# Optimization experiments

Measured on AMD Instinct MI355X. Metric: run time of the kernel, lower is better.

Reference implementation:

```python
import jax, jax.numpy as jnp
import numpy as np

N_NODES = 50000
N_EDGES = 800000
N_GRAPHS = 256
N_FEAT, N_HID, N_EMB = 128, 256, 256
BN_EPS = 1e-5
W_SCALE = 0.05  # keep activations well-scaled through 3 layers


def setup_inputs() -> dict:
    key = jax.random.key(0)
    ks = jax.random.split(key, 9)
    x = jax.random.normal(ks[0], (N_NODES, N_FEAT), jnp.float32)
    edge_index = jax.random.randint(ks[1], (2, N_EDGES), 0, N_NODES)
    batch = jnp.sort(jax.random.randint(ks[2], (N_NODES,), 0, N_GRAPHS))
    return {
        "x": x,
        "edge_index": edge_index,
        "batch": batch,
        "W1_0": jax.random.normal(ks[3], (N_FEAT, N_HID), jnp.float32) * W_SCALE,
        "W2_0": jax.random.normal(ks[4], (N_HID, N_HID), jnp.float32) * W_SCALE,
        "gamma0": jnp.ones((N_HID,), jnp.float32),
        "beta0": jnp.zeros((N_HID,), jnp.float32),
        "W1_1": jax.random.normal(ks[5], (N_HID, N_HID), jnp.float32) * W_SCALE,
        "W2_1": jax.random.normal(ks[6], (N_HID, N_HID), jnp.float32) * W_SCALE,
        "gamma1": jnp.ones((N_HID,), jnp.float32),
        "beta1": jnp.zeros((N_HID,), jnp.float32),
        "W1_2": jax.random.normal(ks[7], (N_HID, N_HID), jnp.float32) * W_SCALE,
        "W2_2": jax.random.normal(ks[8], (N_HID, N_EMB), jnp.float32) * W_SCALE,
    }


def _gin_conv(x, src, dst, W1, W2):
    # PyG GINConv, eps=0: nn((1+eps)*x_i + sum_{j in N(i)} x_j)
    agg = jax.ops.segment_sum(x[src], dst, num_segments=N_NODES)  # [N, d]
    h = x + agg
    return jax.nn.relu(h @ W1) @ W2  # Linear(bias=False) -> act -> Linear(bias=False)


def _batch_norm(h, gamma, beta):
    # BatchNorm1d in training mode: biased batch stats over nodes
    mean = jnp.mean(h, axis=0)
    var = jnp.var(h, axis=0)
    return (h - mean) * jax.lax.rsqrt(var + BN_EPS) * gamma + beta


def reference(x, edge_index, batch, W1_0, W2_0, gamma0, beta0,
              W1_1, W2_1, gamma1, beta1, W1_2, W2_2):
    src, dst = edge_index[0], edge_index[1]
    layers = [(W1_0, W2_0, gamma0, beta0), (W1_1, W2_1, gamma1, beta1)]
    xs = []
    h = x
    for W1, W2, g, b in layers:  # n_layers-1 conv+act+BN blocks
        h = jax.nn.relu(_gin_conv(h, src, dst, W1, W2))
        h = _batch_norm(h, g, b)
        xs.append(h)
    h = _gin_conv(h, src, dst, W1_2, W2_2)  # final conv: no act, no BN
    xs.append(h)
    xpool = jax.ops.segment_sum(h, batch, num_segments=N_GRAPHS)  # global_add_pool
    return xpool, jnp.concatenate(xs, axis=1)
```

## Files before the change

### kernel.cpp

```cpp
#include <hip/hip_runtime.h>
#include <stdint.h>

typedef unsigned int u32;
typedef unsigned short u16;

using s16x8 = __attribute__((ext_vector_type(8))) short;
using f32x4 = __attribute__((ext_vector_type(4))) float;

#define N_NODES_C 50000
#define N_EDGES_C 800000
#define N_GRAPHS_C 256
#define N_FEAT_C 128
#define N_HID_C 256

static __device__ __forceinline__ float bf2f(u16 u) {
  union { u32 u; float f; } c; c.u = ((u32)u) << 16; return c.f;
}
static __device__ __forceinline__ u16 f2bf(float f) {
  union { float f; u32 u; } c; c.f = f;
  u32 u = c.u;
  return (u16)((u + 0x7fffu + ((u >> 16) & 1u)) >> 16);
}

static __device__ __forceinline__ void gload_lds16(const u16* g, u16* l) {
  __builtin_amdgcn_global_load_lds(
      (const __attribute__((address_space(1))) unsigned int*)g,
      (__attribute__((address_space(3))) unsigned int*)l, 16, 0, 0);
}

__global__ void convt_all_kernel(const float* __restrict__ Wa, const float* __restrict__ Wb,
                                 const float* __restrict__ Wc, const float* __restrict__ Wd,
                                 const float* __restrict__ We, const float* __restrict__ Wf,
                                 u16* oa, u16* ob, u16* oc, u16* od, u16* oe, u16* of_) {
  int m = blockIdx.y;
  const float* W; u16* o; int K;
  switch (m) {
    case 0: W = Wa; o = oa; K = 128; break;
    case 1: W = Wb; o = ob; K = 256; break;
    case 2: W = Wc; o = oc; K = 256; break;
    case 3: W = Wd; o = od; K = 256; break;
    case 4: W = We; o = oe; K = 256; break;
    default: W = Wf; o = of_; K = 256; break;
  }
  int idx = blockIdx.x * 256 + threadIdx.x;
  if (idx >= K * 256) return;
  int n = idx / K, k = idx - n * K;
  o[idx] = f2bf(W[(size_t)k * 256 + n]);
}

__global__ void cvt4_kernel(const float* __restrict__ x, u16* __restrict__ xb, int n4) {
  int idx = blockIdx.x * 256 + threadIdx.x;
  if (idx >= n4) return;
  float4 v = reinterpret_cast<const float4*>(x)[idx];
  u32 lo = (u32)f2bf(v.x) | ((u32)f2bf(v.y) << 16);
  u32 hi = (u32)f2bf(v.z) | ((u32)f2bf(v.w) << 16);
  uint2 w; w.x = lo; w.y = hi;
  reinterpret_cast<uint2*>(xb)[idx] = w;
}

__global__ void count_kernel(const int* __restrict__ dst, int* __restrict__ cnt, int E) {
  int e = blockIdx.x * 256 + threadIdx.x;
  if (e < E) atomicAdd(&cnt[dst[e]], 1);
}

__global__ void scanA_kernel(const int* __restrict__ cnt, int* __restrict__ incl,
                             int* __restrict__ bsum, int n) {
  __shared__ int sd[1024];
  int i = blockIdx.x * 1024 + (int)threadIdx.x;
  int v = (i < n) ? cnt[i] : 0;
  sd[threadIdx.x] = v;
  __syncthreads();
  for (int off = 1; off < 1024; off <<= 1) {
    int t = ((int)threadIdx.x >= off) ? sd[threadIdx.x - off] : 0;
    __syncthreads();
    sd[threadIdx.x] += t;
    __syncthreads();
  }
  if (i < n) incl[i] = sd[threadIdx.x];
  if (threadIdx.x == 1023) bsum[blockIdx.x] = sd[1023];
}

__global__ void scanB_kernel(int* bsum, int nb, float* stats0, float* stats1) {
  int t = threadIdx.x;
  for (int i = t; i < 512; i += 64) { stats0[i] = 0.f; stats1[i] = 0.f; }
  if (t == 0) {
    int s = 0;
    for (int b = 0; b < nb; b++) { int v = bsum[b]; bsum[b] = s; s += v; }
  }
}

__global__ void scanC_kernel(const int* __restrict__ cnt, const int* __restrict__ incl,
                             const int* __restrict__ bsum, int* __restrict__ offs,
                             int* __restrict__ cursor, int n) {
  int i = blockIdx.x * 1024 + (int)threadIdx.x;
  if (i < n) {
    int e = incl[i] - cnt[i] + bsum[blockIdx.x];
    offs[i] = e;
    cursor[i] = e;
  }
  if (i == 0) offs[n] = N_EDGES_C;
}

__global__ void fill_kernel(const int* __restrict__ src, const int* __restrict__ dst,
                            int* __restrict__ cursor, int* __restrict__ csr, int E) {
  int e = blockIdx.x * 256 + threadIdx.x;
  if (e < E) {
    int p = atomicAdd(&cursor[dst[e]], 1);
    csr[p] = src[e];
  }
}

template <int D, bool AFFINE>
__global__ __launch_bounds__(256) void agg_kernel(const u16* __restrict__ xin,
                                                  const int* __restrict__ offs,
                                                  const int* __restrict__ csr,
                                                  const float* __restrict__ sb,
                                                  u16* __restrict__ hout) {
  constexpr int LPE = D / 8;
  constexpr int EPW = 64 / LPE;
  int wid = threadIdx.x >> 6, lane = threadIdx.x & 63;
  int node = blockIdx.x * 4 + wid;
  if (node >= N_NODES_C) return;
  int sub = lane / LPE;
  int fl = lane % LPE;
  int f0 = fl * 8;
  float acc[8];
  if (sub == 0) {
    uint4 v = *reinterpret_cast<const uint4*>(xin + (size_t)node * D + f0);
    const u32* pv = reinterpret_cast<const u32*>(&v);
#pragma unroll
    for (int t = 0; t < 4; t++) {
      acc[2 * t] = bf2f((u16)pv[t]);
      acc[2 * t + 1] = bf2f((u16)(pv[t] >> 16));
    }
  } else {
#pragma unroll
    for (int t = 0; t < 8; t++) acc[t] = 0.f;
  }
  int e0 = offs[node];
  int e1 = offs[node + 1];
  int e = e0 + sub;
  if (EPW == 2) {
    for (; e + 3 * EPW < e1; e += 4 * EPW) {
      int s0 = csr[e], s1 = csr[e + EPW], s2 = csr[e + 2 * EPW], s3 = csr[e + 3 * EPW];
      uint4 v0 = *reinterpret_cast<const uint4*>(xin + (size_t)s0 * D + f0);
      uint4 v1 = *reinterpret_cast<const uint4*>(xin + (size_t)s1 * D + f0);
      uint4 v2 = *reinterpret_cast<const uint4*>(xin + (size_t)s2 * D + f0);
      uint4 v3 = *reinterpret_cast<const uint4*>(xin + (size_t)s3 * D + f0);
      const u32* p0 = reinterpret_cast<const u32*>(&v0);
      const u32* p1 = reinterpret_cast<const u32*>(&v1);
      const u32* p2 = reinterpret_cast<const u32*>(&v2);
      const u32* p3 = reinterpret_cast<const u32*>(&v3);
#pragma unroll
      for (int t = 0; t < 4; t++) {
        acc[2 * t] += (bf2f((u16)p0[t]) + bf2f((u16)p1[t])) +
                      (bf2f((u16)p2[t]) + bf2f((u16)p3[t]));
        acc[2 * t + 1] += (bf2f((u16)(p0[t] >> 16)) + bf2f((u16)(p1[t] >> 16))) +
                          (bf2f((u16)(p2[t] >> 16)) + bf2f((u16)(p3[t] >> 16)));
      }
    }
  } else {
    for (; e + EPW < e1; e += 2 * EPW) {
      int s0 = csr[e], s1 = csr[e + EPW];
      uint4 v0 = *reinterpret_cast<const uint4*>(xin + (size_t)s0 * D + f0);
      uint4 v1 = *reinterpret_cast<const uint4*>(xin + (size_t)s1 * D + f0);
      const u32* p0 = reinterpret_cast<const u32*>(&v0);
      const u32* p1 = reinterpret_cast<const u32*>(&v1);
#pragma unroll
      for (int t = 0; t < 4; t++) {
        acc[2 * t] += bf2f((u16)p0[t]) + bf2f((u16)p1[t]);
        acc[2 * t + 1] += bf2f((u16)(p0[t] >> 16)) + bf2f((u16)(p1[t] >> 16));
      }
    }
  }
  for (; e < e1; e += EPW) {
    int s = csr[e];
    uint4 v = *reinterpret_cast<const uint4*>(xin + (size_t)s * D + f0);
    const u32* pv = reinterpret_cast<const u32*>(&v);
#pragma unroll
    for (int t = 0; t < 4; t++) {
      acc[2 * t] += bf2f((u16)pv[t]);
      acc[2 * t + 1] += bf2f((u16)(pv[t] >> 16));
    }
  }
#pragma unroll
  for (int j = 0; j < 8; j++) {
    if (EPW == 4) acc[j] += __shfl_xor(acc[j], 16, 64);
    acc[j] += __shfl_xor(acc[j], 32, 64);
  }
  if (sub == 0) {
    if (AFFINE) {
      float dp1 = (float)(e1 - e0 + 1);
      float4 sca = *reinterpret_cast<const float4*>(sb + f0);
      float4 scb = *reinterpret_cast<const float4*>(sb + f0 + 4);
      float4 bia = *reinterpret_cast<const float4*>(sb + 256 + f0);
      float4 bib = *reinterpret_cast<const float4*>(sb + 256 + f0 + 4);
      float sc[8] = {sca.x, sca.y, sca.z, sca.w, scb.x, scb.y, scb.z, scb.w};
      float bi[8] = {bia.x, bia.y, bia.z, bia.w, bib.x, bib.y, bib.z, bib.w};
#pragma unroll
      for (int j = 0; j < 8; j++) acc[j] = fmaf(acc[j], sc[j], bi[j] * dp1);
    }
    u32 w[4];
#pragma unroll
    for (int t = 0; t < 4; t++)
      w[t] = (u32)f2bf(acc[2 * t]) | ((u32)f2bf(acc[2 * t + 1]) << 16);
    *reinterpret_cast<uint4*>(hout + (size_t)node * D + f0) =
        *reinterpret_cast<const uint4*>(w);
  }
}

template <int K, bool RELU, bool OUTF32, bool STATS>
__global__ __launch_bounds__(512, 2) void gemm_kernel(const u16* __restrict__ A,
                                                      const u16* __restrict__ Bt,
                                                      u16* __restrict__ outB,
                                                      float* __restrict__ outF, int ldc,
                                                      float* __restrict__ statsp) {
  constexpr int BM = 128, BK = 64;
  __shared__ u16 Al[BM * BK];
  __shared__ u16 Bl[256 * BK];
  const int tid = threadIdx.x;
  const int wid = tid >> 6, lane = tid & 63;
  const int brow = blockIdx.x * BM;
  const int wr = (wid >> 2) * 64;
  const int wc = (wid & 3) * 64;
  f32x4 acc[4][4] = {};

  const int lrow = lane >> 3;
  const int lw = lane & 7;
  const int colA = (lw ^ lrow) * 8;
  const int sw = (lane & 7) << 3;

  for (int k0 = 0; k0 < K; k0 += BK) {
#pragma unroll
    for (int i = 0; i < 6; i++) {
      int c = wid * 6 + i;
      if (c < 16) {
        int r = c * 8 + lrow;
        int gr = brow + r;
        gr = gr < N_NODES_C ? gr : N_NODES_C - 1;
        gload_lds16(A + (size_t)gr * K + k0 + colA, &Al[c * 512]);
      } else {
        int cc = c - 16;
        int r = cc * 8 + lrow;
        gload_lds16(Bt + (size_t)r * K + k0 + colA, &Bl[cc * 512]);
      }
    }
    __syncthreads();
#pragma unroll
    for (int ks = 0; ks < BK; ks += 32) {
      const int kk = ks + (lane >> 4) * 8;
      const int ki = kk ^ sw;
      s16x8 a[4], b[4];
#pragma unroll
      for (int m = 0; m < 4; m++)
        a[m] = *reinterpret_cast<const s16x8*>(&Al[(wr + m * 16 + (lane & 15)) * 64 + ki]);
#pragma unroll
      for (int n = 0; n < 4; n++)
        b[n] = *reinterpret_cast<const s16x8*>(&Bl[(wc + n * 16 + (lane & 15)) * 64 + ki]);
#pragma unroll
      for (int m = 0; m < 4; m++)
#pragma unroll
        for (int n = 0; n < 4; n++)
          acc[m][n] = __builtin_amdgcn_mfma_f32_16x16x32_bf16(a[m], b[n], acc[m][n], 0, 0, 0);
    }
    __syncthreads();
  }

  const int cb = wc + (lane & 15);
  const int rsub = (lane >> 4) * 4;
  float s1[4] = {0.f, 0.f, 0.f, 0.f}, s2[4] = {0.f, 0.f, 0.f, 0.f};
#pragma unroll
  for (int m = 0; m < 4; m++) {
#pragma unroll
    for (int r = 0; r < 4; r++) {
      int row = brow + wr + m * 16 + rsub + r;
      if (row >= N_NODES_C) continue;
#pragma unroll
      for (int n = 0; n < 4; n++) {
        float v = acc[m][n][r];
        if (RELU) v = v > 0.f ? v : 0.f;
        int col = cb + n * 16;
        if (OUTF32)
          outF[(size_t)row * ldc + col] = v;
        else
          outB[(size_t)row * ldc + col] = f2bf(v);
        if (STATS) { s1[n] += v; s2[n] += v * v; }
      }
    }
  }
  if (STATS) {
#pragma unroll
    for (int n = 0; n < 4; n++) {
      float a0 = s1[n], b0 = s2[n];
      a0 += __shfl_xor(a0, 16, 64);
      b0 += __shfl_xor(b0, 16, 64);
      a0 += __shfl_xor(a0, 32, 64);
      b0 += __shfl_xor(b0, 32, 64);
      if (lane < 16) {
        atomicAdd(&statsp[cb + n * 16], a0);
        atomicAdd(&statsp[256 + cb + n * 16], b0);
      }
    }
  }
}

__global__ __launch_bounds__(256) void norm_kernel(const u16* __restrict__ xp,
                                                   const float* __restrict__ stats,
                                                   const float* __restrict__ gamma,
                                                   const float* __restrict__ beta,
                                                   float* __restrict__ cout,
                                                   float* __restrict__ sb) {
  const float invM = 1.0f / (float)N_NODES_C;
  int f0 = (threadIdx.x & 127) * 2;
  int half = threadIdx.x >> 7;
  float m0 = stats[f0] * invM, m1 = stats[f0 + 1] * invM;
  float v0 = stats[256 + f0] * invM - m0 * m0;
  float v1 = stats[256 + f0 + 1] * invM - m1 * m1;
  float sc0 = gamma[f0] * rsqrtf(v0 + 1e-5f);
  float sc1 = gamma[f0 + 1] * rsqrtf(v1 + 1e-5f);
  float bi0 = beta[f0] - m0 * sc0;
  float bi1 = beta[f0 + 1] - m1 * sc1;
  if (blockIdx.x == 0 && half == 0) {
    sb[f0] = sc0; sb[f0 + 1] = sc1;
    sb[256 + f0] = bi0; sb[256 + f0 + 1] = bi1;
  }
  for (int r = blockIdx.x * 2 + half; r < N_NODES_C; r += 2 * gridDim.x) {
    u32 w = *reinterpret_cast<const u32*>(xp + (size_t)r * 256 + f0);
    float y0 = fmaf(bf2f((u16)w), sc0, bi0);
    float y1 = fmaf(bf2f((u16)(w >> 16)), sc1, bi1);
    float2 y; y.x = y0; y.y = y1;
    *reinterpret_cast<float2*>(cout + (size_t)r * 768 + f0) = y;
  }
}

__global__ __launch_bounds__(256) void pool_kernel(const float* __restrict__ c, int ldc,
                                                   const int* __restrict__ batch,
                                                   float* __restrict__ outp) {
  __shared__ float red[1024];
  int g = blockIdx.x;
  int wid = threadIdx.x >> 6, lane = threadIdx.x & 63;
  int lo = 0, hi = N_NODES_C;
  while (lo < hi) { int mid = (lo + hi) >> 1; if (batch[mid] < g) lo = mid + 1; else hi = mid; }
  int start = lo;
  hi = N_NODES_C;
  while (lo < hi) { int mid = (lo + hi) >> 1; if (batch[mid] <= g) lo = mid + 1; else hi = mid; }
  int end = lo;
  float acc[4] = {0.f, 0.f, 0.f, 0.f};
  for (int r = start + wid; r < end; r += 4) {
    float4 v = *reinterpret_cast<const float4*>(c + (size_t)r * ldc + lane * 4);
    acc[0] += v.x; acc[1] += v.y; acc[2] += v.z; acc[3] += v.w;
  }
#pragma unroll
  for (int j = 0; j < 4; j++) red[wid * 256 + lane * 4 + j] = acc[j];
  __syncthreads();
  int f = threadIdx.x;
  float s = red[f] + red[256 + f] + red[512 + f] + red[768 + f];
  outp[(size_t)g * 256 + f] = s;
}

extern "C" void kernel_launch(void* const* d_in, const int* in_sizes, int n_in,
                              void* d_out, int out_size, void* d_ws, size_t ws_size,
                              hipStream_t stream) {
  (void)in_sizes; (void)n_in; (void)out_size; (void)ws_size;
  const float* x = (const float*)d_in[0];
  const int* ei = (const int*)d_in[1];
  const int* batch = (const int*)d_in[2];
  const float* W1_0 = (const float*)d_in[3];
  const float* W2_0 = (const float*)d_in[4];
  const float* gamma0 = (const float*)d_in[5];
  const float* beta0 = (const float*)d_in[6];
  const float* W1_1 = (const float*)d_in[7];
  const float* W2_1 = (const float*)d_in[8];
  const float* gamma1 = (const float*)d_in[9];
  const float* beta1 = (const float*)d_in[10];
  const float* W1_2 = (const float*)d_in[11];
  const float* W2_2 = (const float*)d_in[12];

  float* out = (float*)d_out;
  float* xpool = out;
  float* concat = out + (size_t)N_GRAPHS_C * N_HID_C;

  char* ws = (char*)d_ws;
  size_t off = 0;
  auto alloc = [&](size_t bytes) -> char* {
    char* p = ws + off;
    off = (off + bytes + 255) & ~(size_t)255;
    return p;
  };
  int* cnt = (int*)alloc((N_NODES_C + 1) * 4);
  int* offs = (int*)alloc((N_NODES_C + 1) * 4);
  int* cursor = (int*)alloc(N_NODES_C * 4);
  int* incl = (int*)alloc(N_NODES_C * 4);
  int* bsum = (int*)alloc(64 * 4);
  int* csr = (int*)alloc((size_t)N_EDGES_C * 4);
  u16* xb = (u16*)alloc((size_t)N_NODES_C * N_FEAT_C * 2);
  u16* hin = (u16*)alloc((size_t)N_NODES_C * N_HID_C * 2);
  u16* tbuf = (u16*)alloc((size_t)N_NODES_C * N_HID_C * 2);
  u16* hpre = (u16*)alloc((size_t)N_NODES_C * N_HID_C * 2);
  u16* w10t = (u16*)alloc((size_t)N_FEAT_C * N_HID_C * 2);
  u16* w20t = (u16*)alloc((size_t)N_HID_C * N_HID_C * 2);
  u16* w11t = (u16*)alloc((size_t)N_HID_C * N_HID_C * 2);
  u16* w21t = (u16*)alloc((size_t)N_HID_C * N_HID_C * 2);
  u16* w12t = (u16*)alloc((size_t)N_HID_C * N_HID_C * 2);
  u16* w22t = (u16*)alloc((size_t)N_HID_C * N_HID_C * 2);
  float* stats0 = (float*)alloc(512 * 4);
  float* stats1 = (float*)alloc(512 * 4);
  float* sb0 = (float*)alloc(512 * 4);
  float* sb1 = (float*)alloc(512 * 4);

  const int* srcv = ei;
  const int* dstv = ei + N_EDGES_C;
  const int nb = (N_NODES_C + 1023) / 1024;
  const int ggrid = (N_NODES_C + 127) / 128;

  hipMemsetAsync(cnt, 0, (N_NODES_C + 1) * 4, stream);

  convt_all_kernel<<<dim3(256, 6), 256, 0, stream>>>(W1_0, W2_0, W1_1, W2_1, W1_2, W2_2,
                                                     w10t, w20t, w11t, w21t, w12t, w22t);
  cvt4_kernel<<<(N_NODES_C * N_FEAT_C / 4 + 255) / 256, 256, 0, stream>>>(
      x, xb, N_NODES_C * N_FEAT_C / 4);

  count_kernel<<<(N_EDGES_C + 255) / 256, 256, 0, stream>>>(dstv, cnt, N_EDGES_C);
  scanA_kernel<<<nb, 1024, 0, stream>>>(cnt, incl, bsum, N_NODES_C);
  scanB_kernel<<<1, 64, 0, stream>>>(bsum, nb, stats0, stats1);
  scanC_kernel<<<nb, 1024, 0, stream>>>(cnt, incl, bsum, offs, cursor, N_NODES_C);
  fill_kernel<<<(N_EDGES_C + 255) / 256, 256, 0, stream>>>(srcv, dstv, cursor, csr, N_EDGES_C);

  agg_kernel<128, false><<<(N_NODES_C + 3) / 4, 256, 0, stream>>>(xb, offs, csr, nullptr, hin);
  gemm_kernel<128, true, false, false><<<ggrid, 512, 0, stream>>>(hin, w10t, tbuf, nullptr, N_HID_C, nullptr);
  gemm_kernel<256, true, false, true><<<ggrid, 512, 0, stream>>>(tbuf, w20t, hpre, nullptr, N_HID_C, stats0);
  norm_kernel<<<2048, 256, 0, stream>>>(hpre, stats0, gamma0, beta0, concat + 0, sb0);

  agg_kernel<256, true><<<(N_NODES_C + 3) / 4, 256, 0, stream>>>(hpre, offs, csr, sb0, hin);
  gemm_kernel<256, true, false, false><<<ggrid, 512, 0, stream>>>(hin, w11t, tbuf, nullptr, N_HID_C, nullptr);
  gemm_kernel<256, true, false, true><<<ggrid, 512, 0, stream>>>(tbuf, w21t, hpre, nullptr, N_HID_C, stats1);
  norm_kernel<<<2048, 256, 0, stream>>>(hpre, stats1, gamma1, beta1, concat + 256, sb1);

  agg_kernel<256, true><<<(N_NODES_C + 3) / 4, 256, 0, stream>>>(hpre, offs, csr, sb1, hin);
  gemm_kernel<256, true, false, false><<<ggrid, 512, 0, stream>>>(hin, w12t, tbuf, nullptr, N_HID_C, nullptr);
  gemm_kernel<256, false, true, false><<<ggrid, 512, 0, stream>>>(tbuf, w22t, nullptr, concat + 512, 768, nullptr);

  pool_kernel<<<N_GRAPHS_C, 256, 0, stream>>>(concat + 512, 768, batch, xpool);
}
```

Measured before the change: 455.2 us.

## Fuse aggregation, both GEMMs, BN stats and normalization into one kernel per layer

Each GIN layer now runs as a single kernel. The kernel aggregates neighbor features for 128 nodes straight into LDS, runs the first GEMM with double-buffered weight tiles, writes ReLU output back to LDS, and runs the second GEMM. The last block to finish computes the BN scale and bias, and the following layer writes the normalized concat output as it reads its own rows. The three-kernel scan becomes one decoupled-lookback scan, and the memsets are folded into the weight-conversion kernel. This drops the intermediate global buffers and many launches, but uses 80KB of LDS per block, which lowers occupancy, and relies on spin-waiting across blocks.

```diff
diff --git a/kernel.cpp b/kernel.cpp
--- a/kernel.cpp
+++ b/kernel.cpp
@@ -31,8 +31,18 @@
 __global__ void convt_all_kernel(const float* __restrict__ Wa, const float* __restrict__ Wb,
                                  const float* __restrict__ Wc, const float* __restrict__ Wd,
                                  const float* __restrict__ We, const float* __restrict__ Wf,
-                                 u16* oa, u16* ob, u16* oc, u16* od, u16* oe, u16* of_) {
+                                 u16* oa, u16* ob, u16* oc, u16* od, u16* oe, u16* of_,
+                                 int* cnt, int* flags, int* donecnt,
+                                 float* stats0, float* stats1) {
   int m = blockIdx.y;
+  if (m == 6) {
+    int idx = blockIdx.x * 256 + threadIdx.x;
+    if (idx <= N_NODES_C) cnt[idx] = 0;
+    if (idx < 64) flags[idx] = 0;
+    if (idx < 2) donecnt[idx] = 0;
+    if (idx < 512) { stats0[idx] = 0.f; stats1[idx] = 0.f; }
+    return;
+  }
   const float* W; u16* o; int K;
   switch (m) {
     case 0: W = Wa; o = oa; K = 128; break;
@@ -63,10 +73,12 @@
   if (e < E) atomicAdd(&cnt[dst[e]], 1);
 }
 
-__global__ void scanA_kernel(const int* __restrict__ cnt, int* __restrict__ incl,
-                             int* __restrict__ bsum, int n) {
+__global__ void scan_fused_kernel(const int* __restrict__ cnt, int* __restrict__ offs,
+                                  int* __restrict__ cursor, int* __restrict__ flags, int n) {
   __shared__ int sd[1024];
-  int i = blockIdx.x * 1024 + (int)threadIdx.x;
+  __shared__ int prefix_sh;
+  int b = blockIdx.x;
+  int i = b * 1024 + (int)threadIdx.x;
   int v = (i < n) ? cnt[i] : 0;
   sd[threadIdx.x] = v;
   __syncthreads();
@@ -76,29 +88,21 @@
     sd[threadIdx.x] += t;
     __syncthreads();
   }
-  if (i < n) incl[i] = sd[threadIdx.x];
-  if (threadIdx.x == 1023) bsum[blockIdx.x] = sd[1023];
-}
-
-__global__ void scanB_kernel(int* bsum, int nb, float* stats0, float* stats1) {
-  int t = threadIdx.x;
-  for (int i = t; i < 512; i += 64) { stats0[i] = 0.f; stats1[i] = 0.f; }
-  if (t == 0) {
-    int s = 0;
-    for (int b = 0; b < nb; b++) { int v = bsum[b]; bsum[b] = s; s += v; }
-  }
-}
-
-__global__ void scanC_kernel(const int* __restrict__ cnt, const int* __restrict__ incl,
-                             const int* __restrict__ bsum, int* __restrict__ offs,
-                             int* __restrict__ cursor, int n) {
-  int i = blockIdx.x * 1024 + (int)threadIdx.x;
-  if (i < n) {
-    int e = incl[i] - cnt[i] + bsum[blockIdx.x];
-    offs[i] = e;
-    cursor[i] = e;
-  }
-  if (i == 0) offs[n] = N_EDGES_C;
+  if (threadIdx.x == 0) {
+    int total = sd[1023];
+    atomicExch(&flags[b], (total << 1) | 1);
+    int p = 0;
+    for (int j = 0; j < b; j++) {
+      int f;
+      do { f = atomicAdd(&flags[j], 0); } while (!(f & 1));
+      p += (f >> 1);
+    }
+    prefix_sh = p;
+  }
+  __syncthreads();
+  int excl = sd[threadIdx.x] - v + prefix_sh;
+  if (i < n) { offs[i] = excl; cursor[i] = excl; }
+  if (i == n) offs[n] = N_EDGES_C;
 }
 
 __global__ void fill_kernel(const int* __restrict__ src, const int* __restrict__ dst,
@@ -110,185 +114,239 @@
   }
 }
 
-template <int D, bool AFFINE>
-__global__ __launch_bounds__(256) void agg_kernel(const u16* __restrict__ xin,
-                                                  const int* __restrict__ offs,
-                                                  const int* __restrict__ csr,
-                                                  const float* __restrict__ sb,
-                                                  u16* __restrict__ hout) {
-  constexpr int LPE = D / 8;
-  constexpr int EPW = 64 / LPE;
-  int wid = threadIdx.x >> 6, lane = threadIdx.x & 63;
-  int node = blockIdx.x * 4 + wid;
-  if (node >= N_NODES_C) return;
-  int sub = lane / LPE;
-  int fl = lane % LPE;
-  int f0 = fl * 8;
-  float acc[8];
-  if (sub == 0) {
-    uint4 v = *reinterpret_cast<const uint4*>(xin + (size_t)node * D + f0);
-    const u32* pv = reinterpret_cast<const u32*>(&v);
-#pragma unroll
-    for (int t = 0; t < 4; t++) {
-      acc[2 * t] = bf2f((u16)pv[t]);
-      acc[2 * t + 1] = bf2f((u16)(pv[t] >> 16));
-    }
-  } else {
-#pragma unroll
-    for (int t = 0; t < 8; t++) acc[t] = 0.f;
-  }
-  int e0 = offs[node];
-  int e1 = offs[node + 1];
-  int e = e0 + sub;
-  if (EPW == 2) {
-    for (; e + 3 * EPW < e1; e += 4 * EPW) {
-      int s0 = csr[e], s1 = csr[e + EPW], s2 = csr[e + 2 * EPW], s3 = csr[e + 3 * EPW];
-      uint4 v0 = *reinterpret_cast<const uint4*>(xin + (size_t)s0 * D + f0);
-      uint4 v1 = *reinterpret_cast<const uint4*>(xin + (size_t)s1 * D + f0);
-      uint4 v2 = *reinterpret_cast<const uint4*>(xin + (size_t)s2 * D + f0);
-      uint4 v3 = *reinterpret_cast<const uint4*>(xin + (size_t)s3 * D + f0);
-      const u32* p0 = reinterpret_cast<const u32*>(&v0);
-      const u32* p1 = reinterpret_cast<const u32*>(&v1);
-      const u32* p2 = reinterpret_cast<const u32*>(&v2);
-      const u32* p3 = reinterpret_cast<const u32*>(&v3);
-#pragma unroll
-      for (int t = 0; t < 4; t++) {
-        acc[2 * t] += (bf2f((u16)p0[t]) + bf2f((u16)p1[t])) +
-                      (bf2f((u16)p2[t]) + bf2f((u16)p3[t]));
-        acc[2 * t + 1] += (bf2f((u16)(p0[t] >> 16)) + bf2f((u16)(p1[t] >> 16))) +
-                          (bf2f((u16)(p2[t] >> 16)) + bf2f((u16)(p3[t] >> 16)));
-      }
-    }
-  } else {
-    for (; e + EPW < e1; e += 2 * EPW) {
-      int s0 = csr[e], s1 = csr[e + EPW];
-      uint4 v0 = *reinterpret_cast<const uint4*>(xin + (size_t)s0 * D + f0);
-      uint4 v1 = *reinterpret_cast<const uint4*>(xin + (size_t)s1 * D + f0);
-      const u32* p0 = reinterpret_cast<const u32*>(&v0);
-      const u32* p1 = reinterpret_cast<const u32*>(&v1);
-#pragma unroll
-      for (int t = 0; t < 4; t++) {
-        acc[2 * t] += bf2f((u16)p0[t]) + bf2f((u16)p1[t]);
-        acc[2 * t + 1] += bf2f((u16)(p0[t] >> 16)) + bf2f((u16)(p1[t] >> 16));
-      }
-    }
-  }
-  for (; e < e1; e += EPW) {
-    int s = csr[e];
-    uint4 v = *reinterpret_cast<const uint4*>(xin + (size_t)s * D + f0);
-    const u32* pv = reinterpret_cast<const u32*>(&v);
-#pragma unroll
-    for (int t = 0; t < 4; t++) {
-      acc[2 * t] += bf2f((u16)pv[t]);
-      acc[2 * t + 1] += bf2f((u16)(pv[t] >> 16));
-    }
-  }
-#pragma unroll
-  for (int j = 0; j < 8; j++) {
-    if (EPW == 4) acc[j] += __shfl_xor(acc[j], 16, 64);
-    acc[j] += __shfl_xor(acc[j], 32, 64);
-  }
-  if (sub == 0) {
-    if (AFFINE) {
-      float dp1 = (float)(e1 - e0 + 1);
-      float4 sca = *reinterpret_cast<const float4*>(sb + f0);
-      float4 scb = *reinterpret_cast<const float4*>(sb + f0 + 4);
-      float4 bia = *reinterpret_cast<const float4*>(sb + 256 + f0);
-      float4 bib = *reinterpret_cast<const float4*>(sb + 256 + f0 + 4);
-      float sc[8] = {sca.x, sca.y, sca.z, sca.w, scb.x, scb.y, scb.z, scb.w};
-      float bi[8] = {bia.x, bia.y, bia.z, bia.w, bib.x, bib.y, bib.z, bib.w};
-#pragma unroll
-      for (int j = 0; j < 8; j++) acc[j] = fmaf(acc[j], sc[j], bi[j] * dp1);
-    }
-    u32 w[4];
-#pragma unroll
-    for (int t = 0; t < 4; t++)
-      w[t] = (u32)f2bf(acc[2 * t]) | ((u32)f2bf(acc[2 * t + 1]) << 16);
-    *reinterpret_cast<uint4*>(hout + (size_t)node * D + f0) =
-        *reinterpret_cast<const uint4*>(w);
-  }
-}
-
-template <int K, bool RELU, bool OUTF32, bool STATS>
-__global__ __launch_bounds__(512, 2) void gemm_kernel(const u16* __restrict__ A,
-                                                      const u16* __restrict__ Bt,
-                                                      u16* __restrict__ outB,
-                                                      float* __restrict__ outF, int ldc,
-                                                      float* __restrict__ statsp) {
-  constexpr int BM = 128, BK = 64;
-  __shared__ u16 Al[BM * BK];
-  __shared__ u16 Bl[256 * BK];
+template <int K1, bool AFFINE, bool LAST>
+__global__ __launch_bounds__(512) void layer_kernel(
+    const u16* __restrict__ xin, const int* __restrict__ offs, const int* __restrict__ csr,
+    const float* __restrict__ sbin, float* __restrict__ concat_prev,
+    const u16* __restrict__ w1t, const u16* __restrict__ w2t,
+    u16* __restrict__ hout, float* __restrict__ cout,
+    float* __restrict__ statsp, const float* __restrict__ gamma,
+    const float* __restrict__ beta, float* __restrict__ sbout, int* __restrict__ donecnt) {
+  __shared__ u16 Al[128 * 256];
+  __shared__ u16 Wb[2][256 * 64];
+  __shared__ int amlast;
   const int tid = threadIdx.x;
   const int wid = tid >> 6, lane = tid & 63;
-  const int brow = blockIdx.x * BM;
+  const int brow = blockIdx.x * 128;
+
+  auto stageW = [&](const u16* Wt, int stride, int k0, int bufi) {
+    const int lrow = lane >> 3, lw = lane & 7;
+    const int colA = (lw ^ lrow) * 8;
+#pragma unroll
+    for (int i = 0; i < 4; i++) {
+      int c = wid * 4 + i;
+      int r = c * 8 + lrow;
+      gload_lds16(Wt + (size_t)r * stride + k0 + colA, &Wb[bufi][c * 512]);
+    }
+  };
+
+  stageW(w1t, K1, 0, 0);
+
+  {
+    constexpr int LPE = K1 / 8;
+    constexpr int EPW = 64 / LPE;
+    const int sub = lane / LPE;
+    const int fl = lane % LPE;
+    const int f0 = fl * 8;
+    for (int i = 0; i < 16; i++) {
+      int r = wid * 16 + i;
+      int node = brow + r;
+      bool real = node < N_NODES_C;
+      int nd = real ? node : N_NODES_C - 1;
+      float acc[8], own[8];
+      if (sub == 0) {
+        uint4 v = *reinterpret_cast<const uint4*>(xin + (size_t)nd * K1 + f0);
+        const u32* pv = reinterpret_cast<const u32*>(&v);
+#pragma unroll
+        for (int t = 0; t < 4; t++) {
+          acc[2 * t] = bf2f((u16)pv[t]);
+          acc[2 * t + 1] = bf2f((u16)(pv[t] >> 16));
+          own[2 * t] = acc[2 * t];
+          own[2 * t + 1] = acc[2 * t + 1];
+        }
+      } else {
+#pragma unroll
+        for (int t = 0; t < 8; t++) acc[t] = 0.f;
+      }
+      int e0 = offs[nd], e1 = offs[nd + 1];
+      int e = e0 + sub;
+      if (EPW == 2) {
+        for (; e + 3 * EPW < e1; e += 4 * EPW) {
+          int s0 = csr[e], s1 = csr[e + EPW], s2 = csr[e + 2 * EPW], s3 = csr[e + 3 * EPW];
+          uint4 v0 = *reinterpret_cast<const uint4*>(xin + (size_t)s0 * K1 + f0);
+          uint4 v1 = *reinterpret_cast<const uint4*>(xin + (size_t)s1 * K1 + f0);
+          uint4 v2 = *reinterpret_cast<const uint4*>(xin + (size_t)s2 * K1 + f0);
+          uint4 v3 = *reinterpret_cast<const uint4*>(xin + (size_t)s3 * K1 + f0);
+          const u32* p0 = reinterpret_cast<const u32*>(&v0);
+          const u32* p1 = reinterpret_cast<const u32*>(&v1);
+          const u32* p2 = reinterpret_cast<const u32*>(&v2);
+          const u32* p3 = reinterpret_cast<const u32*>(&v3);
+#pragma unroll
+          for (int t = 0; t < 4; t++) {
+            acc[2 * t] += (bf2f((u16)p0[t]) + bf2f((u16)p1[t])) +
+                          (bf2f((u16)p2[t]) + bf2f((u16)p3[t]));
+            acc[2 * t + 1] += (bf2f((u16)(p0[t] >> 16)) + bf2f((u16)(p1[t] >> 16))) +
+                              (bf2f((u16)(p2[t] >> 16)) + bf2f((u16)(p3[t] >> 16)));
+          }
+        }
+      } else {
+        for (; e + EPW < e1; e += 2 * EPW) {
+          int s0 = csr[e], s1 = csr[e + EPW];
+          uint4 v0 = *reinterpret_cast<const uint4*>(xin + (size_t)s0 * K1 + f0);
+          uint4 v1 = *reinterpret_cast<const uint4*>(xin + (size_t)s1 * K1 + f0);
+          const u32* p0 = reinterpret_cast<const u32*>(&v0);
+          const u32* p1 = reinterpret_cast<const u32*>(&v1);
+#pragma unroll
+          for (int t = 0; t < 4; t++) {
+            acc[2 * t] += bf2f((u16)p0[t]) + bf2f((u16)p1[t]);
+            acc[2 * t + 1] += bf2f((u16)(p0[t] >> 16)) + bf2f((u16)(p1[t] >> 16));
+          }
+        }
+      }
+      for (; e < e1; e += EPW) {
+        int s = csr[e];
+        uint4 v = *reinterpret_cast<const uint4*>(xin + (size_t)s * K1 + f0);
+        const u32* pv = reinterpret_cast<const u32*>(&v);
+#pragma unroll
+        for (int t = 0; t < 4; t++) {
+          acc[2 * t] += bf2f((u16)pv[t]);
+          acc[2 * t + 1] += bf2f((u16)(pv[t] >> 16));
+        }
+      }
+#pragma unroll
+      for (int j = 0; j < 8; j++) {
+        if (EPW == 4) acc[j] += __shfl_xor(acc[j], 16, 64);
+        acc[j] += __shfl_xor(acc[j], 32, 64);
+      }
+      if (sub == 0) {
+        if (AFFINE) {
+          float4 sca = *reinterpret_cast<const float4*>(sbin + f0);
+          float4 scb = *reinterpret_cast<const float4*>(sbin + f0 + 4);
+          float4 bia = *reinterpret_cast<const float4*>(sbin + 256 + f0);
+          float4 bib = *reinterpret_cast<const float4*>(sbin + 256 + f0 + 4);
+          float sc[8] = {sca.x, sca.y, sca.z, sca.w, scb.x, scb.y, scb.z, scb.w};
+          float bi[8] = {bia.x, bia.y, bia.z, bia.w, bib.x, bib.y, bib.z, bib.w};
+          if (real) {
+            float4 y0, y1;
+            y0.x = fmaf(own[0], sc[0], bi[0]); y0.y = fmaf(own[1], sc[1], bi[1]);
+            y0.z = fmaf(own[2], sc[2], bi[2]); y0.w = fmaf(own[3], sc[3], bi[3]);
+            y1.x = fmaf(own[4], sc[4], bi[4]); y1.y = fmaf(own[5], sc[5], bi[5]);
+            y1.z = fmaf(own[6], sc[6], bi[6]); y1.w = fmaf(own[7], sc[7], bi[7]);
+            *reinterpret_cast<float4*>(concat_prev + (size_t)node * 768 + f0) = y0;
+            *reinterpret_cast<float4*>(concat_prev + (size_t)node * 768 + f0 + 4) = y1;
+          }
+          float dp1 = (float)(e1 - e0 + 1);
+#pragma unroll
+          for (int j = 0; j < 8; j++) acc[j] = fmaf(acc[j], sc[j], bi[j] * dp1);
+        }
+        u32 w[4];
+#pragma unroll
+        for (int t = 0; t < 4; t++)
+          w[t] = (u32)f2bf(acc[2 * t]) | ((u32)f2bf(acc[2 * t + 1]) << 16);
+        int swz = (fl & ~7) | ((fl & 7) ^ (r & 7));
+        *reinterpret_cast<uint4*>(&Al[r * K1 + swz * 8]) =
+            *reinterpret_cast<const uint4*>(w);
+      }
+    }
+  }
+  __syncthreads();
+
+  constexpr int S1 = K1 / 64;
   const int wr = (wid >> 2) * 64;
   const int wc = (wid & 3) * 64;
-  f32x4 acc[4][4] = {};
-
-  const int lrow = lane >> 3;
-  const int lw = lane & 7;
-  const int colA = (lw ^ lrow) * 8;
+  const int l15 = lane & 15;
   const int sw = (lane & 7) << 3;
-
-  for (int k0 = 0; k0 < K; k0 += BK) {
-#pragma unroll
-    for (int i = 0; i < 6; i++) {
-      int c = wid * 6 + i;
-      if (c < 16) {
-        int r = c * 8 + lrow;
-        int gr = brow + r;
-        gr = gr < N_NODES_C ? gr : N_NODES_C - 1;
-        gload_lds16(A + (size_t)gr * K + k0 + colA, &Al[c * 512]);
-      } else {
-        int cc = c - 16;
-        int r = cc * 8 + lrow;
-        gload_lds16(Bt + (size_t)r * K + k0 + colA, &Bl[cc * 512]);
-      }
-    }
-    __syncthreads();
-#pragma unroll
-    for (int ks = 0; ks < BK; ks += 32) {
+  f32x4 acc1[4][4] = {};
+#pragma unroll
+  for (int t = 0; t < S1; t++) {
+    if (t + 1 < S1) stageW(w1t, K1, (t + 1) * 64, (t + 1) & 1);
+#pragma unroll
+    for (int ks = 0; ks < 64; ks += 32) {
       const int kk = ks + (lane >> 4) * 8;
       const int ki = kk ^ sw;
       s16x8 a[4], b[4];
 #pragma unroll
       for (int m = 0; m < 4; m++)
-        a[m] = *reinterpret_cast<const s16x8*>(&Al[(wr + m * 16 + (lane & 15)) * 64 + ki]);
+        a[m] = *reinterpret_cast<const s16x8*>(&Al[(wr + m * 16 + l15) * K1 + t * 64 + ki]);
 #pragma unroll
       for (int n = 0; n < 4; n++)
-        b[n] = *reinterpret_cast<const s16x8*>(&Bl[(wc + n * 16 + (lane & 15)) * 64 + ki]);
+        b[n] = *reinterpret_cast<const s16x8*>(&Wb[t & 1][(wc + n * 16 + l15) * 64 + ki]);
 #pragma unroll
       for (int m = 0; m < 4; m++)
 #pragma unroll
         for (int n = 0; n < 4; n++)
-          acc[m][n] = __builtin_amdgcn_mfma_f32_16x16x32_bf16(a[m], b[n], acc[m][n], 0, 0, 0);
+          acc1[m][n] = __builtin_amdgcn_mfma_f32_16x16x32_bf16(a[m], b[n], acc1[m][n], 0, 0, 0);
     }
     __syncthreads();
   }
 
-  const int cb = wc + (lane & 15);
-  const int rsub = (lane >> 4) * 4;
-  float s1[4] = {0.f, 0.f, 0.f, 0.f}, s2[4] = {0.f, 0.f, 0.f, 0.f};
-#pragma unroll
-  for (int m = 0; m < 4; m++) {
-#pragma unroll
-    for (int r = 0; r < 4; r++) {
-      int row = brow + wr + m * 16 + rsub + r;
-      if (row >= N_NODES_C) continue;
-#pragma unroll
-      for (int n = 0; n < 4; n++) {
-        float v = acc[m][n][r];
-        if (RELU) v = v > 0.f ? v : 0.f;
-        int col = cb + n * 16;
-        if (OUTF32)
-          outF[(size_t)row * ldc + col] = v;
-        else
-          outB[(size_t)row * ldc + col] = f2bf(v);
-        if (STATS) { s1[n] += v; s2[n] += v * v; }
-      }
-    }
-  }
-  if (STATS) {
+  stageW(w2t, 256, 0, 0);
+
+  {
+    const int rs = (lane >> 4) * 4;
+#pragma unroll
+    for (int m = 0; m < 4; m++) {
+#pragma unroll
+      for (int rr = 0; rr < 4; rr++) {
+        int row = wr + m * 16 + rs + rr;
+#pragma unroll
+        for (int n = 0; n < 4; n++) {
+          int col = wc + n * 16 + l15;
+          float v = acc1[m][n][rr];
+          v = v > 0.f ? v : 0.f;
+          int slot = col >> 3;
+          int swz = (slot & ~7) | ((slot & 7) ^ (row & 7));
+          Al[row * 256 + swz * 8 + (col & 7)] = f2bf(v);
+        }
+      }
+    }
+  }
+  __syncthreads();
+
+  f32x4 acc2[4][4] = {};
+#pragma unroll
+  for (int t = 0; t < 4; t++) {
+    if (t + 1 < 4) stageW(w2t, 256, (t + 1) * 64, (t + 1) & 1);
+#pragma unroll
+    for (int ks = 0; ks < 64; ks += 32) {
+      const int kk = ks + (lane >> 4) * 8;
+      const int ki = kk ^ sw;
+      s16x8 a[4], b[4];
+#pragma unroll
+      for (int m = 0; m < 4; m++)
+        a[m] = *reinterpret_cast<const s16x8*>(&Al[(wr + m * 16 + l15) * 256 + t * 64 + ki]);
+#pragma unroll
+      for (int n = 0; n < 4; n++)
+        b[n] = *reinterpret_cast<const s16x8*>(&Wb[t & 1][(wc + n * 16 + l15) * 64 + ki]);
+#pragma unroll
+      for (int m = 0; m < 4; m++)
+#pragma unroll
+        for (int n = 0; n < 4; n++)
+          acc2[m][n] = __builtin_amdgcn_mfma_f32_16x16x32_bf16(a[m], b[n], acc2[m][n], 0, 0, 0);
+    }
+    __syncthreads();
+  }
+
+  const int cb = wc + l15;
+  const int rs = (lane >> 4) * 4;
+  if constexpr (!LAST) {
+    float s1[4] = {0.f, 0.f, 0.f, 0.f}, s2[4] = {0.f, 0.f, 0.f, 0.f};
+#pragma unroll
+    for (int m = 0; m < 4; m++) {
+#pragma unroll
+      for (int rr = 0; rr < 4; rr++) {
+        int row = brow + wr + m * 16 + rs + rr;
+        if (row >= N_NODES_C) continue;
+#pragma unroll
+        for (int n = 0; n < 4; n++) {
+          float v = acc2[m][n][rr];
+          v = v > 0.f ? v : 0.f;
+          hout[(size_t)row * 256 + cb + n * 16] = f2bf(v);
+          s1[n] += v;
+          s2[n] += v * v;
+        }
+      }
+    }
 #pragma unroll
     for (int n = 0; n < 4; n++) {
       float a0 = s1[n], b0 = s2[n];
@@ -301,35 +359,32 @@
         atomicAdd(&statsp[256 + cb + n * 16], b0);
       }
     }
-  }
-}
-
-__global__ __launch_bounds__(256) void norm_kernel(const u16* __restrict__ xp,
-                                                   const float* __restrict__ stats,
-                                                   const float* __restrict__ gamma,
-                                                   const float* __restrict__ beta,
-                                                   float* __restrict__ cout,
-                                                   float* __restrict__ sb) {
-  const float invM = 1.0f / (float)N_NODES_C;
-  int f0 = (threadIdx.x & 127) * 2;
-  int half = threadIdx.x >> 7;
-  float m0 = stats[f0] * invM, m1 = stats[f0 + 1] * invM;
-  float v0 = stats[256 + f0] * invM - m0 * m0;
-  float v1 = stats[256 + f0 + 1] * invM - m1 * m1;
-  float sc0 = gamma[f0] * rsqrtf(v0 + 1e-5f);
-  float sc1 = gamma[f0 + 1] * rsqrtf(v1 + 1e-5f);
-  float bi0 = beta[f0] - m0 * sc0;
-  float bi1 = beta[f0 + 1] - m1 * sc1;
-  if (blockIdx.x == 0 && half == 0) {
-    sb[f0] = sc0; sb[f0 + 1] = sc1;
-    sb[256 + f0] = bi0; sb[256 + f0 + 1] = bi1;
-  }
-  for (int r = blockIdx.x * 2 + half; r < N_NODES_C; r += 2 * gridDim.x) {
-    u32 w = *reinterpret_cast<const u32*>(xp + (size_t)r * 256 + f0);
-    float y0 = fmaf(bf2f((u16)w), sc0, bi0);
-    float y1 = fmaf(bf2f((u16)(w >> 16)), sc1, bi1);
-    float2 y; y.x = y0; y.y = y1;
-    *reinterpret_cast<float2*>(cout + (size_t)r * 768 + f0) = y;
+    __threadfence();
+    if (tid == 0) amlast = (atomicAdd(donecnt, 1) == (int)gridDim.x - 1) ? 1 : 0;
+    __syncthreads();
+    if (amlast && tid < 256) {
+      int f = tid;
+      const float invM = 1.0f / (float)N_NODES_C;
+      float s = atomicAdd(&statsp[f], 0.0f);
+      float sq = atomicAdd(&statsp[256 + f], 0.0f);
+      float mean = s * invM;
+      float var = sq * invM - mean * mean;
+      float sc = gamma[f] * rsqrtf(var + 1e-5f);
+      sbout[f] = sc;
+      sbout[256 + f] = beta[f] - mean * sc;
+    }
+  } else {
+#pragma unroll
+    for (int m = 0; m < 4; m++) {
+#pragma unroll
+      for (int rr = 0; rr < 4; rr++) {
+        int row = brow + wr + m * 16 + rs + rr;
+        if (row >= N_NODES_C) continue;
+#pragma unroll
+        for (int n = 0; n < 4; n++)
+          cout[(size_t)row * 768 + cb + n * 16] = acc2[m][n][rr];
+      }
+    }
   }
 }
 
@@ -390,13 +445,12 @@
   int* cnt = (int*)alloc((N_NODES_C + 1) * 4);
   int* offs = (int*)alloc((N_NODES_C + 1) * 4);
   int* cursor = (int*)alloc(N_NODES_C * 4);
-  int* incl = (int*)alloc(N_NODES_C * 4);
-  int* bsum = (int*)alloc(64 * 4);
+  int* flags = (int*)alloc(64 * 4);
+  int* donecnt = (int*)alloc(2 * 4);
   int* csr = (int*)alloc((size_t)N_EDGES_C * 4);
   u16* xb = (u16*)alloc((size_t)N_NODES_C * N_FEAT_C * 2);
-  u16* hin = (u16*)alloc((size_t)N_NODES_C * N_HID_C * 2);
-  u16* tbuf = (u16*)alloc((size_t)N_NODES_C * N_HID_C * 2);
-  u16* hpre = (u16*)alloc((size_t)N_NODES_C * N_HID_C * 2);
+  u16* hpreA = (u16*)alloc((size_t)N_NODES_C * N_HID_C * 2);
+  u16* hpreB = (u16*)alloc((size_t)N_NODES_C * N_HID_C * 2);
   u16* w10t = (u16*)alloc((size_t)N_FEAT_C * N_HID_C * 2);
   u16* w20t = (u16*)alloc((size_t)N_HID_C * N_HID_C * 2);
   u16* w11t = (u16*)alloc((size_t)N_HID_C * N_HID_C * 2);
@@ -411,34 +465,27 @@
   const int* srcv = ei;
   const int* dstv = ei + N_EDGES_C;
   const int nb = (N_NODES_C + 1023) / 1024;
-  const int ggrid = (N_NODES_C + 127) / 128;
-
-  hipMemsetAsync(cnt, 0, (N_NODES_C + 1) * 4, stream);
-
-  convt_all_kernel<<<dim3(256, 6), 256, 0, stream>>>(W1_0, W2_0, W1_1, W2_1, W1_2, W2_2,
-                                                     w10t, w20t, w11t, w21t, w12t, w22t);
+  const int lgrid = (N_NODES_C + 127) / 128;
+
+  convt_all_kernel<<<dim3(256, 7), 256, 0, stream>>>(
+      W1_0, W2_0, W1_1, W2_1, W1_2, W2_2, w10t, w20t, w11t, w21t, w12t, w22t,
+      cnt, flags, donecnt, stats0, stats1);
   cvt4_kernel<<<(N_NODES_C * N_FEAT_C / 4 + 255) / 256, 256, 0, stream>>>(
       x, xb, N_NODES_C * N_FEAT_C / 4);
 
   count_kernel<<<(N_EDGES_C + 255) / 256, 256, 0, stream>>>(dstv, cnt, N_EDGES_C);
-  scanA_kernel<<<nb, 1024, 0, stream>>>(cnt, incl, bsum, N_NODES_C);
-  scanB_kernel<<<1, 64, 0, stream>>>(bsum, nb, stats0, stats1);
-  scanC_kernel<<<nb, 1024, 0, stream>>>(cnt, incl, bsum, offs, cursor, N_NODES_C);
+  scan_fused_kernel<<<nb, 1024, 0, stream>>>(cnt, offs, cursor, flags, N_NODES_C);
   fill_kernel<<<(N_EDGES_C + 255) / 256, 256, 0, stream>>>(srcv, dstv, cursor, csr, N_EDGES_C);
 
-  agg_kernel<128, false><<<(N_NODES_C + 3) / 4, 256, 0, stream>>>(xb, offs, csr, nullptr, hin);
-  gemm_kernel<128, true, false, false><<<ggrid, 512, 0, stream>>>(hin, w10t, tbuf, nullptr, N_HID_C, nullptr);
-  gemm_kernel<256, true, false, true><<<ggrid, 512, 0, stream>>>(tbuf, w20t, hpre, nullptr, N_HID_C, stats0);
-  norm_kernel<<<2048, 256, 0, stream>>>(hpre, stats0, gamma0, beta0, concat + 0, sb0);
-
-  agg_kernel<256, true><<<(N_NODES_C + 3) / 4, 256, 0, stream>>>(hpre, offs, csr, sb0, hin);
-  gemm_kernel<256, true, false, false><<<ggrid, 512, 0, stream>>>(hin, w11t, tbuf, nullptr, N_HID_C, nullptr);
-  gemm_kernel<256, true, false, true><<<ggrid, 512, 0, stream>>>(tbuf, w21t, hpre, nullptr, N_HID_C, stats1);
-  norm_kernel<<<2048, 256, 0, stream>>>(hpre, stats1, gamma1, beta1, concat + 256, sb1);
-
-  agg_kernel<256, true><<<(N_NODES_C + 3) / 4, 256, 0, stream>>>(hpre, offs, csr, sb1, hin);
-  gemm_kernel<256, true, false, false><<<ggrid, 512, 0, stream>>>(hin, w12t, tbuf, nullptr, N_HID_C, nullptr);
-  gemm_kernel<256, false, true, false><<<ggrid, 512, 0, stream>>>(tbuf, w22t, nullptr, concat + 512, 768, nullptr);
+  layer_kernel<128, false, false><<<lgrid, 512, 0, stream>>>(
+      xb, offs, csr, nullptr, nullptr, w10t, w20t, hpreA, nullptr,
+      stats0, gamma0, beta0, sb0, donecnt);
+  layer_kernel<256, true, false><<<lgrid, 512, 0, stream>>>(
+      hpreA, offs, csr, sb0, concat + 0, w11t, w21t, hpreB, nullptr,
+      stats1, gamma1, beta1, sb1, donecnt + 1);
+  layer_kernel<256, true, true><<<lgrid, 512, 0, stream>>>(
+      hpreB, offs, csr, sb1, concat + 256, w12t, w22t, nullptr, concat + 512,
+      nullptr, nullptr, nullptr, nullptr, nullptr);
 
   pool_kernel<<<N_GRAPHS_C, 256, 0, stream>>>(concat + 512, 768, batch, xpool);
 }
```

Result: slower. 780.6 us (+71.5%).

## Fuse BN output write into aggregation and collapse scan into single-pass kernel

Applied to the files above, without the earlier changes.

Replaces the three-kernel prefix scan with one kernel that uses per-block flags for decoupled look-back. The memset and stats zeroing move into an extra grid row of the weight conversion kernel. The full norm pass is replaced by a one-block scale/bias kernel, and the normalized fp32 concat output is now written by the next aggregation kernel while it reads the node's own row. This removes several launches and one full read of the bf16 hidden tensor per layer. The look-back spin relies on earlier blocks being resident, which is safe with 49 blocks but is a forward-progress assumption.

```diff
diff --git a/kernel.cpp b/kernel.cpp
--- a/kernel.cpp
+++ b/kernel.cpp
@@ -31,8 +31,16 @@
 __global__ void convt_all_kernel(const float* __restrict__ Wa, const float* __restrict__ Wb,
                                  const float* __restrict__ Wc, const float* __restrict__ Wd,
                                  const float* __restrict__ We, const float* __restrict__ Wf,
-                                 u16* oa, u16* ob, u16* oc, u16* od, u16* oe, u16* of_) {
+                                 u16* oa, u16* ob, u16* oc, u16* od, u16* oe, u16* of_,
+                                 int* cnt, int* flags, float* stats0, float* stats1) {
   int m = blockIdx.y;
+  if (m == 6) {
+    int idx = blockIdx.x * 256 + threadIdx.x;
+    if (idx <= N_NODES_C) cnt[idx] = 0;
+    if (idx < 64) flags[idx] = 0;
+    if (idx < 512) { stats0[idx] = 0.f; stats1[idx] = 0.f; }
+    return;
+  }
   const float* W; u16* o; int K;
   switch (m) {
     case 0: W = Wa; o = oa; K = 128; break;
@@ -63,10 +71,12 @@
   if (e < E) atomicAdd(&cnt[dst[e]], 1);
 }
 
-__global__ void scanA_kernel(const int* __restrict__ cnt, int* __restrict__ incl,
-                             int* __restrict__ bsum, int n) {
+__global__ void scan_fused_kernel(const int* __restrict__ cnt, int* __restrict__ offs,
+                                  int* __restrict__ cursor, int* __restrict__ flags, int n) {
   __shared__ int sd[1024];
-  int i = blockIdx.x * 1024 + (int)threadIdx.x;
+  __shared__ int prefix_sh;
+  int b = blockIdx.x;
+  int i = b * 1024 + (int)threadIdx.x;
   int v = (i < n) ? cnt[i] : 0;
   sd[threadIdx.x] = v;
   __syncthreads();
@@ -76,29 +86,21 @@
     sd[threadIdx.x] += t;
     __syncthreads();
   }
-  if (i < n) incl[i] = sd[threadIdx.x];
-  if (threadIdx.x == 1023) bsum[blockIdx.x] = sd[1023];
-}
-
-__global__ void scanB_kernel(int* bsum, int nb, float* stats0, float* stats1) {
-  int t = threadIdx.x;
-  for (int i = t; i < 512; i += 64) { stats0[i] = 0.f; stats1[i] = 0.f; }
-  if (t == 0) {
-    int s = 0;
-    for (int b = 0; b < nb; b++) { int v = bsum[b]; bsum[b] = s; s += v; }
-  }
-}
-
-__global__ void scanC_kernel(const int* __restrict__ cnt, const int* __restrict__ incl,
-                             const int* __restrict__ bsum, int* __restrict__ offs,
-                             int* __restrict__ cursor, int n) {
-  int i = blockIdx.x * 1024 + (int)threadIdx.x;
-  if (i < n) {
-    int e = incl[i] - cnt[i] + bsum[blockIdx.x];
-    offs[i] = e;
-    cursor[i] = e;
-  }
-  if (i == 0) offs[n] = N_EDGES_C;
+  if (threadIdx.x == 0) {
+    int total = sd[1023];
+    atomicExch(&flags[b], (total << 1) | 1);
+    int p = 0;
+    for (int j = 0; j < b; j++) {
+      int f;
+      do { f = atomicAdd(&flags[j], 0); } while (!(f & 1));
+      p += (f >> 1);
+    }
+    prefix_sh = p;
+  }
+  __syncthreads();
+  int excl = sd[threadIdx.x] - v + prefix_sh;
+  if (i < n) { offs[i] = excl; cursor[i] = excl; }
+  if (i == n) offs[n] = N_EDGES_C;
 }
 
 __global__ void fill_kernel(const int* __restrict__ src, const int* __restrict__ dst,
@@ -115,6 +117,7 @@
                                                   const int* __restrict__ offs,
                                                   const int* __restrict__ csr,
                                                   const float* __restrict__ sb,
+                                                  float* __restrict__ concat_prev,
                                                   u16* __restrict__ hout) {
   constexpr int LPE = D / 8;
   constexpr int EPW = 64 / LPE;
@@ -124,7 +127,7 @@
   int sub = lane / LPE;
   int fl = lane % LPE;
   int f0 = fl * 8;
-  float acc[8];
+  float acc[8], own[8];
   if (sub == 0) {
     uint4 v = *reinterpret_cast<const uint4*>(xin + (size_t)node * D + f0);
     const u32* pv = reinterpret_cast<const u32*>(&v);
@@ -132,6 +135,8 @@
     for (int t = 0; t < 4; t++) {
       acc[2 * t] = bf2f((u16)pv[t]);
       acc[2 * t + 1] = bf2f((u16)(pv[t] >> 16));
+      own[2 * t] = acc[2 * t];
+      own[2 * t + 1] = acc[2 * t + 1];
     }
   } else {
 #pragma unroll
@@ -190,13 +195,20 @@
   }
   if (sub == 0) {
     if (AFFINE) {
-      float dp1 = (float)(e1 - e0 + 1);
       float4 sca = *reinterpret_cast<const float4*>(sb + f0);
       float4 scb = *reinterpret_cast<const float4*>(sb + f0 + 4);
       float4 bia = *reinterpret_cast<const float4*>(sb + 256 + f0);
       float4 bib = *reinterpret_cast<const float4*>(sb + 256 + f0 + 4);
       float sc[8] = {sca.x, sca.y, sca.z, sca.w, scb.x, scb.y, scb.z, scb.w};
       float bi[8] = {bia.x, bia.y, bia.z, bia.w, bib.x, bib.y, bib.z, bib.w};
+      float4 y0, y1;
+      y0.x = fmaf(own[0], sc[0], bi[0]); y0.y = fmaf(own[1], sc[1], bi[1]);
+      y0.z = fmaf(own[2], sc[2], bi[2]); y0.w = fmaf(own[3], sc[3], bi[3]);
+      y1.x = fmaf(own[4], sc[4], bi[4]); y1.y = fmaf(own[5], sc[5], bi[5]);
+      y1.z = fmaf(own[6], sc[6], bi[6]); y1.w = fmaf(own[7], sc[7], bi[7]);
+      *reinterpret_cast<float4*>(concat_prev + (size_t)node * 768 + f0) = y0;
+      *reinterpret_cast<float4*>(concat_prev + (size_t)node * 768 + f0 + 4) = y1;
+      float dp1 = (float)(e1 - e0 + 1);
 #pragma unroll
       for (int j = 0; j < 8; j++) acc[j] = fmaf(acc[j], sc[j], bi[j] * dp1);
     }
@@ -304,33 +316,15 @@
   }
 }
 
-__global__ __launch_bounds__(256) void norm_kernel(const u16* __restrict__ xp,
-                                                   const float* __restrict__ stats,
-                                                   const float* __restrict__ gamma,
-                                                   const float* __restrict__ beta,
-                                                   float* __restrict__ cout,
-                                                   float* __restrict__ sb) {
+__global__ void scalebias_kernel(const float* __restrict__ stats, const float* __restrict__ gamma,
+                                 const float* __restrict__ beta, float* __restrict__ sb) {
+  int f = threadIdx.x;
   const float invM = 1.0f / (float)N_NODES_C;
-  int f0 = (threadIdx.x & 127) * 2;
-  int half = threadIdx.x >> 7;
-  float m0 = stats[f0] * invM, m1 = stats[f0 + 1] * invM;
-  float v0 = stats[256 + f0] * invM - m0 * m0;
-  float v1 = stats[256 + f0 + 1] * invM - m1 * m1;
-  float sc0 = gamma[f0] * rsqrtf(v0 + 1e-5f);
-  float sc1 = gamma[f0 + 1] * rsqrtf(v1 + 1e-5f);
-  float bi0 = beta[f0] - m0 * sc0;
-  float bi1 = beta[f0 + 1] - m1 * sc1;
-  if (blockIdx.x == 0 && half == 0) {
-    sb[f0] = sc0; sb[f0 + 1] = sc1;
-    sb[256 + f0] = bi0; sb[256 + f0 + 1] = bi1;
-  }
-  for (int r = blockIdx.x * 2 + half; r < N_NODES_C; r += 2 * gridDim.x) {
-    u32 w = *reinterpret_cast<const u32*>(xp + (size_t)r * 256 + f0);
-    float y0 = fmaf(bf2f((u16)w), sc0, bi0);
-    float y1 = fmaf(bf2f((u16)(w >> 16)), sc1, bi1);
-    float2 y; y.x = y0; y.y = y1;
-    *reinterpret_cast<float2*>(cout + (size_t)r * 768 + f0) = y;
-  }
+  float mean = stats[f] * invM;
+  float var = stats[256 + f] * invM - mean * mean;
+  float sc = gamma[f] * rsqrtf(var + 1e-5f);
+  sb[f] = sc;
+  sb[256 + f] = beta[f] - mean * sc;
 }
 
 __global__ __launch_bounds__(256) void pool_kernel(const float* __restrict__ c, int ldc,
@@ -390,8 +384,7 @@
   int* cnt = (int*)alloc((N_NODES_C + 1) * 4);
   int* offs = (int*)alloc((N_NODES_C + 1) * 4);
   int* cursor = (int*)alloc(N_NODES_C * 4);
-  int* incl = (int*)alloc(N_NODES_C * 4);
-  int* bsum = (int*)alloc(64 * 4);
+  int* flags = (int*)alloc(64 * 4);
   int* csr = (int*)alloc((size_t)N_EDGES_C * 4);
   u16* xb = (u16*)alloc((size_t)N_NODES_C * N_FEAT_C * 2);
   u16* hin = (u16*)alloc((size_t)N_NODES_C * N_HID_C * 2);
@@ -413,32 +406,38 @@
   const int nb = (N_NODES_C + 1023) / 1024;
   const int ggrid = (N_NODES_C + 127) / 128;
 
-  hipMemsetAsync(cnt, 0, (N_NODES_C + 1) * 4, stream);
-
-  convt_all_kernel<<<dim3(256, 6), 256, 0, stream>>>(W1_0, W2_0, W1_1, W2_1, W1_2, W2_2,
-                                                     w10t, w20t, w11t, w21t, w12t, w22t);
+  convt_all_kernel<<<dim3(256, 7), 256, 0, stream>>>(
+      W1_0, W2_0, W1_1, W2_1, W1_2, W2_2, w10t, w20t, w11t, w21t, w12t, w22t,
+      cnt, flags, stats0, stats1);
   cvt4_kernel<<<(N_NODES_C * N_FEAT_C / 4 + 255) / 256, 256, 0, stream>>>(
       x, xb, N_NODES_C * N_FEAT_C / 4);
 
   count_kernel<<<(N_EDGES_C + 255) / 256, 256, 0, stream>>>(dstv, cnt, N_EDGES_C);
-  scanA_kernel<<<nb, 1024, 0, stream>>>(cnt, incl, bsum, N_NODES_C);
-  scanB_kernel<<<1, 64, 0, stream>>>(bsum, nb, stats0, stats1);
-  scanC_kernel<<<nb, 1024, 0, stream>>>(cnt, incl, bsum, offs, cursor, N_NODES_C);
+  scan_fused_kernel<<<nb, 1024, 0, stream>>>(cnt, offs, cursor, flags, N_NODES_C);
   fill_kernel<<<(N_EDGES_C + 255) / 256, 256, 0, stream>>>(srcv, dstv, cursor, csr, N_EDGES_C);
 
-  agg_kernel<128, false><<<(N_NODES_C + 3) / 4, 256, 0, stream>>>(xb, offs, csr, nullptr, hin);
-  gemm_kernel<128, true, false, false><<<ggrid, 512, 0, stream>>>(hin, w10t, tbuf, nullptr, N_HID_C, nullptr);
-  gemm_kernel<256, true, false, true><<<ggrid, 512, 0, stream>>>(tbuf, w20t, hpre, nullptr, N_HID_C, stats0);
-  norm_kernel<<<2048, 256, 0, stream>>>(hpre, stats0, gamma0, beta0, concat + 0, sb0);
-
-  agg_kernel<256, true><<<(N_NODES_C + 3) / 4, 256, 0, stream>>>(hpre, offs, csr, sb0, hin);
-  gemm_kernel<256, true, false, false><<<ggrid, 512, 0, stream>>>(hin, w11t, tbuf, nullptr, N_HID_C, nullptr);
-  gemm_kernel<256, true, false, true><<<ggrid, 512, 0, stream>>>(tbuf, w21t, hpre, nullptr, N_HID_C, stats1);
-  norm_kernel<<<2048, 256, 0, stream>>>(hpre, stats1, gamma1, beta1, concat + 256, sb1);
-
-  agg_kernel<256, true><<<(N_NODES_C + 3) / 4, 256, 0, stream>>>(hpre, offs, csr, sb1, hin);
-  gemm_kernel<256, true, false, false><<<ggrid, 512, 0, stream>>>(hin, w12t, tbuf, nullptr, N_HID_C, nullptr);
-  gemm_kernel<256, false, true, false><<<ggrid, 512, 0, stream>>>(tbuf, w22t, nullptr, concat + 512, 768, nullptr);
+  agg_kernel<128, false><<<(N_NODES_C + 3) / 4, 256, 0, stream>>>(
+      xb, offs, csr, nullptr, nullptr, hin);
+  gemm_kernel<128, true, false, false><<<ggrid, 512, 0, stream>>>(
+      hin, w10t, tbuf, nullptr, N_HID_C, nullptr);
+  gemm_kernel<256, true, false, true><<<ggrid, 512, 0, stream>>>(
+      tbuf, w20t, hpre, nullptr, N_HID_C, stats0);
+  scalebias_kernel<<<1, 256, 0, stream>>>(stats0, gamma0, beta0, sb0);
+
+  agg_kernel<256, true><<<(N_NODES_C + 3) / 4, 256, 0, stream>>>(
+      hpre, offs, csr, sb0, concat + 0, hin);
+  gemm_kernel<256, true, false, false><<<ggrid, 512, 0, stream>>>(
+      hin, w11t, tbuf, nullptr, N_HID_C, nullptr);
+  gemm_kernel<256, true, false, true><<<ggrid, 512, 0, stream>>>(
+      tbuf, w21t, hpre, nullptr, N_HID_C, stats1);
+  scalebias_kernel<<<1, 256, 0, stream>>>(stats1, gamma1, beta1, sb1);
+
+  agg_kernel<256, true><<<(N_NODES_C + 3) / 4, 256, 0, stream>>>(
+      hpre, offs, csr, sb1, concat + 256, hin);
+  gemm_kernel<256, true, false, false><<<ggrid, 512, 0, stream>>>(
+      hin, w12t, tbuf, nullptr, N_HID_C, nullptr);
+  gemm_kernel<256, false, true, false><<<ggrid, 512, 0, stream>>>(
+      tbuf, w22t, nullptr, concat + 512, 768, nullptr);
 
   pool_kernel<<<N_GRAPHS_C, 256, 0, stream>>>(concat + 512, 768, batch, xpool);
 }
```

Result: faster. 445.9 us (-2.0%).
